# Performance work log

Measured on AMD Instinct MI355X. Metric: run time of the kernel, lower is better.

## Reference

```python
import jax, jax.numpy as jnp
import numpy as np
from jax import lax

DN = ('NCHW', 'OIHW', 'NCHW')
ROUTE_ITERS = 3
CAPS_NUM, OUT_CAPS, OUT_DIM = 8, 10, 16
IN_CAPS_SIZE = 6 * 6 * 32  # 1152


def _squash(u, axis):
    # Faithful to the repo's (buggy but intentional) squash: mod/(1+mod) * (u/mod_sq)
    mod_sq = jnp.sum(u * u, axis=axis, keepdims=True)
    mod = jnp.sqrt(mod_sq)
    return mod / (1.0 + mod) * (u / mod_sq)


def setup_inputs() -> dict:
    key = jax.random.key(0)
    ks = jax.random.split(key, 6)
    return {
        'x': jax.random.normal(ks[0], (180, 1, 28, 28), jnp.float32),
        'conv1_w': jax.random.normal(ks[1], (256, 1, 9, 9), jnp.float32) * 0.05,
        'conv1_b': jax.random.normal(ks[2], (256,), jnp.float32) * 0.05,
        'caps_w': jax.random.normal(ks[3], (8, 32, 256, 9, 9), jnp.float32) * 0.05,
        'caps_b': jax.random.normal(ks[4], (8, 32), jnp.float32) * 0.05,
        'W_route': jax.random.normal(ks[5], (1, 1152, 10, 16, 8), jnp.float32),
    }


def reference(x, conv1_w, conv1_b, caps_w, caps_b, W_route):
    B = x.shape[0]
    # conv1 + relu: [B,1,28,28] -> [B,256,20,20]
    h = lax.conv_general_dilated(x, conv1_w, (1, 1), 'VALID', dimension_numbers=DN)
    h = jax.nn.relu(h + conv1_b[None, :, None, None])
    # 8 capsule convs fused into one grouped-output conv: -> [B, 8*32, 6, 6]
    kw = caps_w.reshape(CAPS_NUM * 32, 256, 9, 9)
    u = lax.conv_general_dilated(h, kw, (2, 2), 'VALID', dimension_numbers=DN)
    u = u + caps_b.reshape(-1)[None, :, None, None]
    u = u.reshape(B, CAPS_NUM, IN_CAPS_SIZE)          # [B,8,1152]
    u = _squash(u, axis=2)
    # Route: u_hat[b,i,o,d] = sum_k W[0,i,o,d,k] * u[b,k,i]
    ut = jnp.swapaxes(u, 1, 2)                         # [B,1152,8]
    u_hat = jnp.einsum('iodk,bik->biod', W_route[0], ut)  # [B,1152,10,16]
    b_ij = jnp.zeros((IN_CAPS_SIZE, OUT_CAPS), u_hat.dtype)
    v = None
    for _ in range(ROUTE_ITERS):
        c_ij = jax.nn.softmax(b_ij, axis=1)            # softmax over out caps
        s = jnp.einsum('io,biod->bod', c_ij, u_hat)    # [B,10,16]
        # Faithful: original squashes s_j over dim=2 == the out-caps axis (10)
        v = _squash(s, axis=1)                         # [B,10,16]
        uv = jnp.einsum('biod,bod->io', u_hat, v) / B  # mean over batch
        b_ij = b_ij + uv
    return v[..., None]                                # [B,10,16,1]
```

## Files before the change

kernel.cpp:

```cpp
#include <hip/hip_runtime.h>
#include <hip/hip_bf16.h>

#define NB 180
typedef __attribute__((ext_vector_type(8))) short short8;
typedef __attribute__((ext_vector_type(4))) float f32x4;
typedef unsigned short ushort_t;

__device__ __forceinline__ void gload16(const void* src, void* lds_base){
    __builtin_amdgcn_global_load_lds(
        (const __attribute__((address_space(1))) unsigned int*)src,
        (__attribute__((address_space(3))) unsigned int*)lds_base, 16, 0, 0);
}

__device__ __forceinline__ ushort_t f2bu(float v){
    __hip_bfloat16 h = __float2bfloat16(v);
    return *(ushort_t*)&h;
}

__global__ __launch_bounds__(256) void build_bpack_t(const float* __restrict__ w,
                                                     __hip_bfloat16* __restrict__ bpack){
    __shared__ float ls[10368];
    int oc = blockIdx.x, ich = blockIdx.y, t = threadIdx.x;
    const float4* src = (const float4*)(w + (size_t)oc * 20736 + ich * 10368);
    for (int i = t; i < 2592; i += 256) ((float4*)ls)[i] = src[i];
    __syncthreads();
    for (int idx = t; idx < 10368; idx += 256){
        int j = idx & 7, icg = (idx >> 3) & 15, kk = idx >> 7;
        bpack[(size_t)(kk * 32 + ich * 16 + icg) * 2048 + oc * 8 + j] =
            __float2bfloat16(ls[(icg * 8 + j) * 81 + kk]);
    }
}

__global__ __launch_bounds__(256) void build_wpack1(const float* __restrict__ w,
                                                    __hip_bfloat16* __restrict__ wpack1){
    int t = blockIdx.x * 256 + threadIdx.x;
    int j = t & 7, oc = (t >> 3) & 255, gg = t >> 11;
    int k = (gg >> 2) * 32 + (gg & 3) * 8 + j;
    float v = (k < 81) ? w[oc * 81 + k] : 0.f;
    wpack1[t] = __float2bfloat16(v);
}

__global__ __launch_bounds__(256) void build_w2(const float* __restrict__ Wr, float* __restrict__ W2){
    __shared__ float ls[15360];
    int i0 = blockIdx.x * 12, t = threadIdx.x;
    const float4* src = (const float4*)(Wr + (size_t)i0 * 1280);
    for (int w = t; w < 3840; w += 256) ((float4*)ls)[w] = src[w];
    __syncthreads();
    for (int idx = t; idx < 15360; idx += 256){
        int d = idx & 15, r = idx >> 4;
        int il = r % 12, ok = r / 12;
        int k = ok & 7, o = ok >> 3;
        W2[(size_t)o * 147456 + (size_t)(k * 1152 + i0 + il) * 16 + d] =
            ls[il * 1280 + o * 128 + d * 8 + k];
    }
}

__global__ __launch_bounds__(256) void conv1_mfma(const float* __restrict__ x,
                                                  const __hip_bfloat16* __restrict__ wpack1,
                                                  const float* __restrict__ bias,
                                                  __hip_bfloat16* __restrict__ hT){
    __shared__ ushort_t xs[784];
    __shared__ ushort_t ktab[96];
    int bid = blockIdx.x;
    int b = bid >> 2, mc = bid & 3;
    int t = threadIdx.x, lane = t & 63, wn = t >> 6;
    int g = lane >> 4, lr = lane & 15;

    for (int i = t; i < 784; i += 256) xs[i] = f2bu(x[b * 784 + i]);
    if (t < 96) ktab[t] = (t < 81) ? (ushort_t)((t / 9) * 28 + (t % 9)) : (ushort_t)0;
    __syncthreads();

    int p0 = mc * 112;
    int pbm[7];
#pragma unroll
    for (int m = 0; m < 7; m++){
        int p = p0 + m * 16 + lr;
        p = p < 400 ? p : 399;
        pbm[m] = (p / 20) * 28 + (p % 20);
    }

    f32x4 acc[7][4];
#pragma unroll
    for (int m = 0; m < 7; m++)
#pragma unroll
        for (int n = 0; n < 4; n++) acc[m][n] = (f32x4){0.f, 0.f, 0.f, 0.f};

#pragma unroll
    for (int ks = 0; ks < 3; ks++){
        short8 ko = *(const short8*)&ktab[ks * 32 + g * 8];
        short8 bf[4];
#pragma unroll
        for (int n = 0; n < 4; n++)
            bf[n] = *(const short8*)(wpack1 + (size_t)(((ks * 4 + g) * 256) + wn * 64 + n * 16 + lr) * 8);
#pragma unroll
        for (int m = 0; m < 7; m++){
            short8 af;
#pragma unroll
            for (int e = 0; e < 8; e++)
                af[e] = (short)xs[pbm[m] + (int)(ushort_t)ko[e]];
#pragma unroll
            for (int n = 0; n < 4; n++)
                acc[m][n] = __builtin_amdgcn_mfma_f32_16x16x32_bf16(af, bf[n], acc[m][n], 0, 0, 0);
        }
    }

    float bv[4];
#pragma unroll
    for (int n = 0; n < 4; n++) bv[n] = bias[wn * 64 + n * 16 + lr];
#pragma unroll
    for (int m = 0; m < 7; m++){
#pragma unroll
        for (int rg = 0; rg < 4; rg++){
            int p = p0 + m * 16 + g * 4 + rg;
            if (p < 400){
#pragma unroll
                for (int n = 0; n < 4; n++){
                    float v = acc[m][n][rg] + bv[n];
                    v = v > 0.f ? v : 0.f;
                    hT[((size_t)b * 400 + p) * 256 + wn * 64 + n * 16 + lr] = __float2bfloat16(v);
                }
            }
        }
    }
}

__global__ __launch_bounds__(256, 2) void capsconv_mfma(const __hip_bfloat16* __restrict__ hT,
                                                        const __hip_bfloat16* __restrict__ bpack,
                                                        float* __restrict__ part){
    extern __shared__ char smem[];
    ushort_t* hsA = (ushort_t*)smem;

    int bid = blockIdx.x;
    int idx = (bid & 7) * 51 + (bid >> 3);
    if (idx >= 405) return;
    int mt = idx / 9, ky = idx - mt * 9;
    int b0 = mt * 4;
    int t = threadIdx.x, lane = t & 63, wn = t >> 6;
    int g = lane >> 4, lr = lane & 15;

    int pfm[9];
#pragma unroll
    for (int m = 0; m < 9; m++){
        int R = m * 16 + lr;
        int lb = R / 36, pos = R - lb * 36;
        int oy = pos / 6, ox = pos - oy * 6;
        int yy = lb * 6 + oy;
        pfm[m] = ((yy * 20 + 2 * ox) << 8) | (ox + 6 * yy);
    }
    int gbase = g * 2048 + wn * 512 + lr * 8;

    auto stageA = [&](int a){
#pragma unroll
        for (int rnd = 0; rnd < 15; rnd++){
            int L = rnd * 256 + t;
            int p = L >> 3, sg = L & 7;
            int yy = p / 20, xx = p - yy * 20;
            int lb = yy / 6;
            int y = ky + 2 * (yy - lb * 6);
            int f = ((xx >> 1) + 6 * yy) & 7;
            const __hip_bfloat16* src = hT + ((size_t)(((b0 + lb) * 20 + y) * 20 + xx) * 256
                                             + a * 64 + 8 * (sg ^ f));
            gload16(src, hsA + (size_t)(rnd * 256 + (t & ~63)) * 8);
        }
    };

    f32x4 acc[9][4];
#pragma unroll
    for (int m = 0; m < 9; m++)
#pragma unroll
        for (int n = 0; n < 4; n++) acc[m][n] = (f32x4){0.f, 0.f, 0.f, 0.f};

    stageA(0);
    __syncthreads();

    for (int a = 0; a < 4; a++){
#pragma unroll 2
        for (int r = 0; r < 18; r++){
            int kx = r >> 1, ics = r & 1;
            int ksg = (ky * 9 + kx) * 8 + 2 * a + ics;
            const __hip_bfloat16* bstep = bpack + (size_t)ksg * 8192 + gbase;
            short8 bf[4];
#pragma unroll
            for (int n = 0; n < 4; n++)
                bf[n] = *(const short8*)(bstep + n * 128);
            int jj = ics * 4 + g;
#pragma unroll
            for (int m = 0; m < 9; m++){
                int pf = pfm[m];
                int p = (pf >> 8) + kx;
                int f = ((pf & 255) + (kx >> 1)) & 7;
                short8 af = *(const short8*)(hsA + (size_t)(p * 8 + (jj ^ f)) * 8);
#pragma unroll
                for (int n = 0; n < 4; n++)
                    acc[m][n] = __builtin_amdgcn_mfma_f32_16x16x32_bf16(af, bf[n], acc[m][n], 0, 0, 0);
            }
        }
        if (a < 3){
            __syncthreads();
            stageA(a + 1);
            __syncthreads();
        }
    }

    float* tl = (float*)smem;
    size_t pbase = ((size_t)ky * 180 + b0) * 9216;
    for (int lb = 0; lb < 4; lb++){
        int rlo = lb * 36;
        __syncthreads();
#pragma unroll
        for (int m = 0; m < 9; m++){
#pragma unroll
            for (int n = 0; n < 4; n++){
                int oc = wn * 64 + n * 16 + lr;
#pragma unroll
                for (int rg = 0; rg < 4; rg++){
                    int row = m * 16 + g * 4 + rg;
                    if (row >= rlo && row < rlo + 36)
                        tl[(row - rlo) * 260 + oc] = acc[m][n][rg];
                }
            }
        }
        __syncthreads();
#pragma unroll
        for (int j = 0; j < 9; j++){
            int pos = j * 4;
            float4 vv;
            vv.x = tl[(pos    ) * 260 + t];
            vv.y = tl[(pos + 1) * 260 + t];
            vv.z = tl[(pos + 2) * 260 + t];
            vv.w = tl[(pos + 3) * 260 + t];
            *(float4*)&part[pbase + (size_t)lb * 9216 + t * 36 + pos] = vv;
        }
    }
}

__global__ __launch_bounds__(192) void reduce_squash(const float* __restrict__ part,
                                                     const float* __restrict__ caps_b,
                                                     float* __restrict__ u){
    __shared__ float red[3];
    int bk = blockIdx.x;
    int b = bk >> 3, k = bk & 7;
    int t = threadIdx.x;
    size_t base = (size_t)k * 1152;
    float vals[6];
    float ssq = 0.f;
#pragma unroll
    for (int j = 0; j < 6; j++){
        int i = t + j * 192;
        int oc = k * 32 + i / 36;
        float v = caps_b[oc];
#pragma unroll
        for (int kyi = 0; kyi < 9; kyi++)
            v += part[(size_t)(kyi * 180 + b) * 9216 + base + i];
        vals[j] = v; ssq += v * v;
    }
#pragma unroll
    for (int off = 32; off; off >>= 1) ssq += __shfl_down(ssq, off, 64);
    if ((t & 63) == 0) red[t >> 6] = ssq;
    __syncthreads();
    float tot = red[0] + red[1] + red[2];
    float scale = 1.f / (sqrtf(tot) + tot);
#pragma unroll
    for (int j = 0; j < 6; j++)
        u[(size_t)b * 9216 + base + t + j * 192] = vals[j] * scale;
}

__global__ __launch_bounds__(1024) void transpose_u(const float* __restrict__ u, float* __restrict__ uT){
    __shared__ float tile[32][33];
    int ki0 = blockIdx.x * 32, b0 = blockIdx.y * 32;
    int tx = threadIdx.x, ty = threadIdx.y;
    int b = b0 + ty;
    if (b < NB) tile[ty][tx] = u[(size_t)b * 9216 + ki0 + tx];
    __syncthreads();
    int bw = b0 + tx;
    if (bw < NB) uT[(size_t)(ki0 + ty) * NB + bw] = tile[tx][ty];
}

__global__ __launch_bounds__(192) void s_partial2(const float* __restrict__ W2, const float* __restrict__ uT,
                                                  const float* __restrict__ bij, float* __restrict__ part72,
                                                  int first){
    __shared__ float ws2[2048];
    __shared__ float cs[128];
    int o = blockIdx.x, kc = blockIdx.y, t = threadIdx.x;
    const float4* src = (const float4*)(W2 + (size_t)o * 147456 + (size_t)kc * 2048);
    for (int w = t; w < 512; w += 192) ((float4*)ws2)[w] = src[w];
    if (t < 128){
        if (first){
            cs[t] = 0.1f;
        } else {
            int ki = kc * 128 + t;
            int i = ki - (ki / 1152) * 1152;
            const float* bp = bij + (size_t)i * 10;
            float v[10]; float mx = -1e30f;
#pragma unroll
            for (int q = 0; q < 10; q++){ v[q] = bp[q]; mx = fmaxf(mx, v[q]); }
            float sum = 0.f;
#pragma unroll
            for (int q = 0; q < 10; q++){ v[q] = __expf(v[q] - mx); sum += v[q]; }
            cs[t] = v[o] / sum;
        }
    }
    __syncthreads();
    if (t < NB){
        f32x4 a0 = {0,0,0,0}, a1 = {0,0,0,0}, a2 = {0,0,0,0}, a3 = {0,0,0,0};
        const float* up = uT + (size_t)kc * 128 * NB + t;
#pragma unroll 4
        for (int j = 0; j < 128; j++){
            float tmp = up[j * NB] * cs[j];
            const f32x4* wp = (const f32x4*)(ws2 + j * 16);
            a0 += tmp * wp[0]; a1 += tmp * wp[1]; a2 += tmp * wp[2]; a3 += tmp * wp[3];
        }
        f32x4* pp = (f32x4*)(part72 + ((size_t)kc * NB + t) * 160 + o * 16);
        pp[0] = a0; pp[1] = a1; pp[2] = a2; pp[3] = a3;
    }
}

__global__ __launch_bounds__(192) void sred_vsq(const float* __restrict__ part72, float* __restrict__ v){
    __shared__ float sv[160];
    __shared__ float sc[16];
    int b = blockIdx.x, t = threadIdx.x;
    float s = 0.f;
    if (t < 160){
        const float* pp = part72 + (size_t)b * 160 + t;
        for (int kc = 0; kc < 72; kc++)
            s += pp[(size_t)kc * NB * 160];
        sv[t] = s;
    }
    __syncthreads();
    if (t < 16){
        float m = 0.f;
#pragma unroll
        for (int o = 0; o < 10; o++){ float x = sv[o * 16 + t]; m += x * x; }
        sc[t] = 1.f / (sqrtf(m) + m);
    }
    __syncthreads();
    if (t < 160) v[b * 160 + t] = s * sc[t & 15];
}

__global__ __launch_bounds__(320) void p_gemm(const float* __restrict__ uT, const float* __restrict__ v,
                                              float* __restrict__ P){
    __shared__ float vs[60 * 160];
    int t = threadIdx.x;
    int o = t % 10, kil = t / 10;
    int ki = blockIdx.x * 32 + kil;
    float acc[16];
#pragma unroll
    for (int d = 0; d < 16; d++) acc[d] = 0.f;
    const float* up = uT + (size_t)ki * NB;
    for (int b0 = 0; b0 < NB; b0 += 60){
        __syncthreads();
        for (int j = t; j < 9600; j += 320) vs[j] = v[b0 * 160 + j];
        __syncthreads();
        for (int b = 0; b < 60; b++){
            float uv = up[b0 + b];
            const float* vp = &vs[b * 160 + o * 16];
#pragma unroll
            for (int d = 0; d < 16; d++) acc[d] += uv * vp[d];
        }
    }
    float* pp = P + (size_t)ki * 160 + o * 16;
#pragma unroll
    for (int d = 0; d < 16; d++) pp[d] = acc[d];
}

__global__ void uv_contract2(const float* __restrict__ W2, const float* __restrict__ P,
                             float* __restrict__ bij, int first){
    int t = blockIdx.x * 256 + threadIdx.x;
    if (t >= 11520) return;
    int o = t % 10, i = t / 10;
    float acc = 0.f;
    for (int k = 0; k < 8; k++){
        const float4* wp = (const float4*)(W2 + (size_t)o * 147456 + (size_t)(k * 1152 + i) * 16);
        const float4* pp = (const float4*)(P + (size_t)(k * 1152 + i) * 160 + o * 16);
#pragma unroll
        for (int q = 0; q < 4; q++){
            float4 a = wp[q], b = pp[q];
            acc += a.x * b.x + a.y * b.y + a.z * b.z + a.w * b.w;
        }
    }
    float val = acc * (1.0f / 180.0f);
    bij[t] = first ? val : bij[t] + val;
}

extern "C" void kernel_launch(void* const* d_in, const int* in_sizes, int n_in,
                              void* d_out, int out_size, void* d_ws, size_t ws_size,
                              hipStream_t stream){
    const float* x       = (const float*)d_in[0];
    const float* conv1_w = (const float*)d_in[1];
    const float* conv1_b = (const float*)d_in[2];
    const float* caps_w  = (const float*)d_in[3];
    const float* caps_b  = (const float*)d_in[4];
    const float* Wr      = (const float*)d_in[5];
    float* out = (float*)d_out;

    char* wsb = (char*)d_ws;
    __hip_bfloat16* hTb   = (__hip_bfloat16*)wsb;
    __hip_bfloat16* bpack = (__hip_bfloat16*)(wsb + 36864000);
    float* part = (float*)(wsb + 36864000 + 10616832);
    float* u    = part + 14929920;
    float* uT   = u + 1658880;
    __hip_bfloat16* wpack1 = (__hip_bfloat16*)((char*)(uT + 1658880));

    float* W2     = part;
    float* part72 = W2 + 1474560;
    float* P      = part72 + 2073600;
    float* bij    = P + 1474560;

    hipFuncSetAttribute((const void*)capsconv_mfma,
                        hipFuncAttributeMaxDynamicSharedMemorySize, 65536);

    build_bpack_t<<<dim3(256, 2), 256, 0, stream>>>(caps_w, bpack);
    build_wpack1<<<96, 256, 0, stream>>>(conv1_w, wpack1);
    conv1_mfma<<<720, 256, 0, stream>>>(x, wpack1, conv1_b, hTb);
    capsconv_mfma<<<408, 256, 61440, stream>>>(hTb, bpack, part);
    reduce_squash<<<1440, 192, 0, stream>>>(part, caps_b, u);
    transpose_u<<<dim3(288, 6), dim3(32, 32), 0, stream>>>(u, uT);
    build_w2<<<96, 256, 0, stream>>>(Wr, W2);

    for (int it = 0; it < 3; ++it){
        s_partial2<<<dim3(10, 72), 192, 0, stream>>>(W2, uT, bij, part72, it == 0 ? 1 : 0);
        sred_vsq<<<180, 192, 0, stream>>>(part72, out);
        if (it < 2){
            p_gemm<<<288, 320, 0, stream>>>(uT, out, P);
            uv_contract2<<<45, 256, 0, stream>>>(W2, P, bij, it == 0 ? 1 : 0);
        }
    }
}
```

Baseline: 307.8 us.

## Double-buffer LDS A tiles and register-prefetch B fragments in capsule conv

The capsule conv MFMA kernel now keeps two LDS buffers for the A (activation) tile. It issues the async global-to-LDS load for the next channel chunk before computing on the current one, which removes one barrier per chunk. B weight fragments are also prefetched one step ahead into registers so global loads overlap with MFMAs. In exchange, dynamic shared memory doubles to 120KB, which limits occupancy to one block per CU, and the extra prefetch registers add VGPR pressure.

```diff
diff --git a/kernel.cpp b/kernel.cpp
--- a/kernel.cpp
+++ b/kernel.cpp
@@ -149,7 +149,8 @@
     }
     int gbase = g * 2048 + wn * 512 + lr * 8;
 
-    auto stageA = [&](int a){
+    auto stageA = [&](int a, int buf){
+        ushort_t* dst = hsA + (size_t)buf * 30720;
 #pragma unroll
         for (int rnd = 0; rnd < 15; rnd++){
             int L = rnd * 256 + t;
@@ -160,9 +161,17 @@
             int f = ((xx >> 1) + 6 * yy) & 7;
             const __hip_bfloat16* src = hT + ((size_t)(((b0 + lb) * 20 + y) * 20 + xx) * 256
                                              + a * 64 + 8 * (sg ^ f));
-            gload16(src, hsA + (size_t)(rnd * 256 + (t & ~63)) * 8);
+            gload16(src, dst + (size_t)(rnd * 256 + (t & ~63)) * 8);
         }
     };
+    auto loadB = [&](int a_, int r_, short8* bf){
+        int kx = r_ >> 1, ics = r_ & 1;
+        int ksg = (ky * 9 + kx) * 8 + 2 * a_ + ics;
+        const __hip_bfloat16* bstep = bpack + (size_t)ksg * 8192 + gbase;
+#pragma unroll
+        for (int n = 0; n < 4; n++)
+            bf[n] = *(const short8*)(bstep + n * 128);
+    };
 
     f32x4 acc[9][4];
 #pragma unroll
@@ -170,36 +179,36 @@
 #pragma unroll
         for (int n = 0; n < 4; n++) acc[m][n] = (f32x4){0.f, 0.f, 0.f, 0.f};
 
-    stageA(0);
-    __syncthreads();
-
+    short8 bcur[4], bnxt[4];
+    stageA(0, 0);
+    loadB(0, 0, bcur);
+    __syncthreads();
+
+#pragma unroll
     for (int a = 0; a < 4; a++){
+        if (a < 3) stageA(a + 1, (a + 1) & 1);
+        const ushort_t* bufA = hsA + (size_t)(a & 1) * 30720;
 #pragma unroll 2
         for (int r = 0; r < 18; r++){
             int kx = r >> 1, ics = r & 1;
-            int ksg = (ky * 9 + kx) * 8 + 2 * a + ics;
-            const __hip_bfloat16* bstep = bpack + (size_t)ksg * 8192 + gbase;
-            short8 bf[4];
-#pragma unroll
-            for (int n = 0; n < 4; n++)
-                bf[n] = *(const short8*)(bstep + n * 128);
+            if (r < 17) loadB(a, r + 1, bnxt);
+            else if (a < 3) loadB(a + 1, 0, bnxt);
             int jj = ics * 4 + g;
 #pragma unroll
             for (int m = 0; m < 9; m++){
                 int pf = pfm[m];
                 int p = (pf >> 8) + kx;
                 int f = ((pf & 255) + (kx >> 1)) & 7;
-                short8 af = *(const short8*)(hsA + (size_t)(p * 8 + (jj ^ f)) * 8);
+                short8 af = *(const short8*)(bufA + (size_t)(p * 8 + (jj ^ f)) * 8);
 #pragma unroll
                 for (int n = 0; n < 4; n++)
-                    acc[m][n] = __builtin_amdgcn_mfma_f32_16x16x32_bf16(af, bf[n], acc[m][n], 0, 0, 0);
+                    acc[m][n] = __builtin_amdgcn_mfma_f32_16x16x32_bf16(af, bcur[n], acc[m][n], 0, 0, 0);
             }
-        }
-        if (a < 3){
+#pragma unroll
+            for (int n = 0; n < 4; n++) bcur[n] = bnxt[n];
+        }
+        if (a < 3)
             __syncthreads();
-            stageA(a + 1);
-            __syncthreads();
-        }
     }
 
     float* tl = (float*)smem;
@@ -407,12 +416,12 @@
     float* bij    = P + 1474560;
 
     hipFuncSetAttribute((const void*)capsconv_mfma,
-                        hipFuncAttributeMaxDynamicSharedMemorySize, 65536);
+                        hipFuncAttributeMaxDynamicSharedMemorySize, 131072);
 
     build_bpack_t<<<dim3(256, 2), 256, 0, stream>>>(caps_w, bpack);
     build_wpack1<<<96, 256, 0, stream>>>(conv1_w, wpack1);
     conv1_mfma<<<720, 256, 0, stream>>>(x, wpack1, conv1_b, hTb);
-    capsconv_mfma<<<408, 256, 61440, stream>>>(hTb, bpack, part);
+    capsconv_mfma<<<408, 256, 122880, stream>>>(hTb, bpack, part);
     reduce_squash<<<1440, 192, 0, stream>>>(part, caps_b, u);
     transpose_u<<<dim3(288, 6), dim3(32, 32), 0, stream>>>(u, uT);
     build_w2<<<96, 256, 0, stream>>>(Wr, W2);
```

After: 349.6 us. +13.6%, slower.
